# Kernel optimization log

Hardware: AMD Instinct MI355X
Metric: run time of the kernel (lower is better)

## Reference

```python
import jax, jax.numpy as jnp
import numpy as np

# Constants matching init_kwargs
PC_MIN_X, PC_MIN_Y = -70.4, -40.0
VX, VY = 0.1, 0.1
RADII = (0.4, 0.8)
NSAMPLE = 16
EPS = 1e-5

B, K, N = 2, 2048, 16384
C_BEV, H_BEV, W_BEV = 256, 100, 176


def setup_inputs() -> dict:
    key = jax.random.key(0)
    ks = jax.random.split(key, 16)
    u = lambda k, s: jax.random.uniform(k, s, jnp.float32)
    kp = jnp.stack([
        u(ks[0], (B, K)) * 136.0 - 68.0,
        u(ks[1], (B, K)) * 76.0 - 38.0,
        u(ks[2], (B, K)) * 2.5 - 2.0,   # z in (-2.0, 0.5) -> kpt_mask all True
    ], axis=-1)
    pts = jnp.stack([
        u(ks[3], (B, N)) * 140.0 - 70.0,
        u(ks[4], (B, N)) * 80.0 - 40.0,
        u(ks[5], (B, N)) * 4.0 - 3.0,
    ], axis=-1)
    r = lambda k, s: jax.random.normal(k, s, jnp.float32)
    s01 = lambda k, s: r(k, s) * 0.1
    return {
        "keypoints": kp,
        "points_xyz": pts,
        "points_feat": r(ks[6], (B, N, 1)),
        "spatial_features": r(ks[7], (B, C_BEV, H_BEV, W_BEV)),
        "bev_stride": 8,
        "W0_s0": s01(ks[8], (16, 4)), "g0_s0": jnp.ones(16), "b0_s0": jnp.zeros(16),
        "W1_s0": s01(ks[9], (16, 16)), "g1_s0": jnp.ones(16), "b1_s0": jnp.zeros(16),
        "W0_s1": s01(ks[10], (16, 4)), "g0_s1": jnp.ones(16), "b0_s1": jnp.zeros(16),
        "W1_s1": s01(ks[11], (32, 16)), "g1_s1": jnp.ones(32), "b1_s1": jnp.zeros(32),
        "Wf": s01(ks[12], (128, 304)), "gf": jnp.ones(128), "bf": jnp.zeros(128),
    }


def _batchnorm(x, g, b, axes):
    m = x.mean(axes, keepdims=True)
    v = x.var(axes, keepdims=True)
    return (x - m) * jax.lax.rsqrt(v + EPS) * g + b


def _ball_group(dist2, xyz_b, feat_b, kp_b, radius, ns):
    """pcdet ball_query: first ns in-radius neighbors (index order), pad by first idx."""
    Kq, Np = dist2.shape
    within = dist2 < radius * radius                      # (K, N)
    order = jnp.cumsum(within, axis=1) - 1                # slot for each point
    valid = within & (order < ns)
    pos = jnp.where(valid, order, ns)                     # invalid -> overflow slot
    idx = jnp.zeros((Kq, ns + 1), jnp.int32)
    idx = idx.at[jnp.arange(Kq)[:, None], pos].set(
        jnp.broadcast_to(jnp.arange(Np, dtype=jnp.int32)[None, :], (Kq, Np)))
    idx = idx[:, :ns]
    cnt = within.sum(axis=1)
    slot_ok = jnp.arange(ns)[None, :] < cnt[:, None]
    idx = jnp.where(slot_ok, idx, idx[:, :1])             # replicate first found idx
    empty = cnt == 0
    grouped_xyz = xyz_b[idx] - kp_b[:, None, :]           # (K, ns, 3)
    grouped = jnp.concatenate([grouped_xyz, feat_b[idx]], axis=-1)  # (K, ns, 3+C)
    grouped = jnp.where(empty[:, None, None], 0.0, grouped)
    return grouped, empty


def _group_both_scales(xyz_b, feat_b, kp_b):
    # pairwise dist computed ONCE, shared across both radii
    dist2 = jnp.sum((kp_b[:, None, :] - xyz_b[None, :, :]) ** 2, axis=-1)  # (K, N)
    g0, e0 = _ball_group(dist2, xyz_b, feat_b, kp_b, RADII[0], NSAMPLE)
    g1, e1 = _ball_group(dist2, xyz_b, feat_b, kp_b, RADII[1], NSAMPLE)
    return g0, e0, g1, e1


def _shared_mlp_pool(grouped, empty, layers):
    x = grouped                                            # (B, K, ns, Cin)
    for (W, g, b) in layers:
        x = jnp.einsum('bknc,oc->bkno', x, W)
        x = _batchnorm(x, g, b, axes=(0, 1, 2))            # BN2d over stacked M*ns
        x = jax.nn.relu(x)
    pooled = x.max(axis=2)                                 # max over ns -> (B, K, Cout)
    return jnp.where(empty[:, :, None], 0.0, pooled)


def _bev_interp(bev, kp, stride):
    # bev: (B, C, H, W); kp: (B, K, 3)
    im = jnp.transpose(bev, (0, 2, 3, 1))                  # (B, H, W, C)
    x = (kp[..., 0] - PC_MIN_X) / VX / stride
    y = (kp[..., 1] - PC_MIN_Y) / VY / stride
    Hh, Ww = im.shape[1], im.shape[2]
    x0 = jnp.clip(jnp.floor(x).astype(jnp.int32), 0, Ww - 1)
    x1 = jnp.clip(jnp.floor(x).astype(jnp.int32) + 1, 0, Ww - 1)
    y0 = jnp.clip(jnp.floor(y).astype(jnp.int32), 0, Hh - 1)
    y1 = jnp.clip(jnp.floor(y).astype(jnp.int32) + 1, 0, Hh - 1)
    bidx = jnp.arange(im.shape[0])[:, None]
    Ia, Ib = im[bidx, y0, x0], im[bidx, y1, x0]
    Ic, Id = im[bidx, y0, x1], im[bidx, y1, x1]
    x0f, x1f = x0.astype(x.dtype), x1.astype(x.dtype)
    y0f, y1f = y0.astype(y.dtype), y1.astype(y.dtype)
    wa = ((x1f - x) * (y1f - y))[..., None]
    wb = ((x1f - x) * (y - y0f))[..., None]
    wc = ((x - x0f) * (y1f - y))[..., None]
    wd = ((x - x0f) * (y - y0f))[..., None]
    return Ia * wa + Ib * wb + Ic * wc + Id * wd           # (B, K, C)


def reference(keypoints, points_xyz, points_feat, spatial_features, bev_stride,
              W0_s0, g0_s0, b0_s0, W1_s0, g1_s0, b1_s0,
              W0_s1, g0_s1, b0_s1, W1_s1, g1_s1, b1_s1,
              Wf, gf, bf):
    Bb, Kk, _ = keypoints.shape
    # BEV bilinear interpolation
    bev_feat = _bev_interp(spatial_features, keypoints, bev_stride)  # (B, K, C_bev)
    # per-batch ball-query grouping (vmapped over batch)
    g0, e0, g1, e1 = jax.vmap(_group_both_scales)(points_xyz, points_feat, keypoints)
    p0 = _shared_mlp_pool(g0, e0, [(W0_s0, g0_s0, b0_s0), (W1_s0, g1_s0, b1_s0)])
    p1 = _shared_mlp_pool(g1, e1, [(W0_s1, g0_s1, b0_s1), (W1_s1, g1_s1, b1_s1)])
    pooled = jnp.concatenate([p0, p1], axis=-1)            # (B, K, 48)
    feats = jnp.concatenate([bev_feat, pooled], axis=-1).reshape(Bb * Kk, -1)  # (M, 304)
    # vsa_point_feature_fusion: Linear(no bias) + BN1d(train) + ReLU
    fused = feats @ Wf.T
    fused = jax.nn.relu(_batchnorm(fused, gf, bf, axes=(0,)))
    return fused                                           # (B*K, 128)
```

## Files before the change

kernel.cpp:

```cpp
#include <hip/hip_runtime.h>
#include <hip/hip_bf16.h>

#define NB    2
#define NK    2048
#define NPTS  16384
#define NBK   4096
#define MSAMP 65536.0f
#define MROW  4096.0f

#define NCELLX 176
#define NCELLY 101
#define NCELLS 17776
#define CAP    24
#define CANDMAX 64

#define NREP   32
#define NCTR   64

#define AL(p) __hip_atomic_load((p), __ATOMIC_RELAXED, __HIP_MEMORY_SCOPE_AGENT)

#define ATOMIC_ADD_ACK(p, v) do { \
  float _r = atomicAdd((p), (v)); \
  asm volatile("" :: "v"(_r)); } while (0)

#define ACC14(M, w, X, Y, Z, F) do { \
  M[0] += (w)*(X); M[1] += (w)*(Y); M[2] += (w)*(Z); M[3] += (w)*(F); \
  M[4] += (w)*(X)*(X); M[5] += (w)*(X)*(Y); M[6] += (w)*(X)*(Z); M[7] += (w)*(X)*(F); \
  M[8] += (w)*(Y)*(Y); M[9] += (w)*(Y)*(Z); M[10] += (w)*(Y)*(F); \
  M[11] += (w)*(Z)*(Z); M[12] += (w)*(Z)*(F); M[13] += (w)*(F)*(F); } while (0)

__device__ __forceinline__ int cell_of(float x, float y) {
  int cx = (int)floorf((x + 70.4f) * 1.25f);
  int cy = (int)floorf((y + 40.0f) * 1.25f);
  cx = min(max(cx, 0), NCELLX - 1);
  cy = min(max(cy, 0), NCELLY - 1);
  return cy * NCELLX + cx;
}

__device__ __forceinline__ void grid_barrier(int* base, int per, int myc) {
  asm volatile("s_waitcnt vmcnt(0)" ::: "memory");
  __syncthreads();
  const int t = threadIdx.x;
  int* ctr = base;
  int* rel = base + NCTR;
  if (t == 0) {
    int old = __hip_atomic_fetch_add(&ctr[myc], 1, __ATOMIC_RELAXED,
                                     __HIP_MEMORY_SCOPE_AGENT);
    asm volatile("" :: "v"(old));
  }
  if (blockIdx.x == 0) {
    if (t < NCTR) {
      while (AL(&ctr[t]) < per) __builtin_amdgcn_s_sleep(8);
    }
    __syncthreads();
    if (t < NCTR)
      __hip_atomic_store(&rel[t], 1, __ATOMIC_RELAXED,
                         __HIP_MEMORY_SCOPE_AGENT);
  } else {
    if (t == 0) {
      while (AL(&rel[myc]) == 0) __builtin_amdgcn_s_sleep(8);
    }
  }
  __syncthreads();
}

__global__ __launch_bounds__(256) void bintrans_kernel(
    const float* __restrict__ pts, const float* __restrict__ pfeat,
    const float* __restrict__ bev,
    int* __restrict__ cellcnt, float4* __restrict__ bucketP,
    int* __restrict__ bucketI, float* __restrict__ bevT)
{
  __shared__ __align__(16) float ttile[64][65];
  const int t = threadIdx.x;
  const int wave = t >> 6;
  const int lane = t & 63;

  if (blockIdx.x < 128) {
    const int i  = blockIdx.x * 256 + t;
    const int b  = i >> 14;
    const int il = i & (NPTS - 1);
    const float* px = pts + (size_t)b * NPTS * 3;
    const float x = px[il*3+0], y = px[il*3+1], z = px[il*3+2];
    const float f = pfeat[(size_t)b * NPTS + il];
    const int c = b * NCELLS + cell_of(x, y);
    const int pos = atomicAdd(&cellcnt[c], 1);
    if (pos < CAP) {
      bucketP[(size_t)c * CAP + pos] = make_float4(x, y, z, f);
      bucketI[(size_t)c * CAP + pos] = il;
    }
    return;
  }

  const int tb  = blockIdx.x - 128;
  const int b   = tb / 1100;
  const int rem = tb % 1100;
  const int cg  = (rem / 275) * 64;
  const int sp0 = (rem % 275) * 64;
  #pragma unroll 4
  for (int i = 0; i < 16; i++) {
    const int c = cg + wave * 16 + i;
    ttile[wave * 16 + i][lane] = bev[((size_t)(b * 256 + c)) * 17600 + sp0 + lane];
  }
  __syncthreads();
  #pragma unroll 4
  for (int i = 0; i < 16; i++) {
    const int s = wave * 16 + i;
    bevT[((size_t)b * 17600 + sp0 + s) * 256 + cg + lane] = ttile[lane][s];
  }
}

__global__ __launch_bounds__(256, 2) void fused_kernel(
    const float* __restrict__ kp, const int* __restrict__ stridep,
    const float* __restrict__ bevT,
    const int* __restrict__ cellcnt, const float4* __restrict__ bucketP,
    const int* __restrict__ bucketI,
    const float* __restrict__ W0s0, const float* __restrict__ gm0s0, const float* __restrict__ bt0s0,
    const float* __restrict__ W0s1, const float* __restrict__ gm0s1, const float* __restrict__ bt0s1,
    const float* __restrict__ W1s0, const float* __restrict__ gm1s0, const float* __restrict__ bt1s0,
    const float* __restrict__ W1s1, const float* __restrict__ gm1s1, const float* __restrict__ bt1s1,
    const float* __restrict__ Wf, const float* __restrict__ gf, const float* __restrict__ bfp,
    float* __restrict__ S0r, float* __restrict__ S1r,
    float* __restrict__ S2sr, float* __restrict__ S2qr,
    int* __restrict__ ctrs, float* __restrict__ out)
{
  __shared__ float sW0a[64], sW0b[64], sW1a[256], sW1b[512], sP[160];
  __shared__ float skp[24];
  __shared__ float red[8][96];
  __shared__ float t2s[2][128], t2q[2][128];
  __shared__ float sA[128], sB[128];
  __shared__ float s0p[8][28], sS0[28];
  __shared__ __align__(16) float sF[8 * 304];
  __shared__ float4 sG0[8][16], sG1[8][16];
  __shared__ __align__(16) float4 sCand[8][CANDMAX];
  __shared__ int sCandI[8][CANDMAX];
  __shared__ int sTot[8];
  __shared__ int scnt[2][8];
  const int t = threadIdx.x;
  const int bk0 = blockIdx.x * 8;
  const int rep = blockIdx.x & (NREP - 1);
  const int myc = blockIdx.x & (NCTR - 1);

  if (t < 24) skp[t] = kp[(size_t)bk0 * 3 + t];
  if (t < 64) { sW0a[t] = W0s0[t]; sW0b[t] = W0s1[t]; }
  sW1a[t]       = W1s0[t];
  sW1b[t]       = W1s1[t];
  sW1b[t + 256] = W1s1[t + 256];
  for (int i = t; i < 8 * 96; i += 256) ((float*)red)[i] = 0.f;
  __syncthreads();

  {
    const float st = (float)(*stridep);
    const int b = bk0 >> 11;
    const size_t pb = (size_t)b * 17600 * 256;
    #pragma unroll
    for (int r = 0; r < 8; r++) {
      const float x = (skp[r*3+0] - (-70.4f)) / 0.1f / st;
      const float y = (skp[r*3+1] - (-40.0f)) / 0.1f / st;
      const int xf = (int)floorf(x), yf = (int)floorf(y);
      const int x0 = min(max(xf, 0), 175), x1 = min(max(xf + 1, 0), 175);
      const int y0 = min(max(yf, 0), 99),  y1 = min(max(yf + 1, 0), 99);
      const float x0f = (float)x0, x1f = (float)x1, y0f = (float)y0, y1f = (float)y1;
      const float wa = (x1f - x) * (y1f - y);
      const float wb = (x1f - x) * (y - y0f);
      const float wc = (x - x0f) * (y1f - y);
      const float wd = (x - x0f) * (y - y0f);
      const float Ia = bevT[pb + (size_t)(y0 * 176 + x0) * 256 + t];
      const float Ib = bevT[pb + (size_t)(y1 * 176 + x0) * 256 + t];
      const float Ic = bevT[pb + (size_t)(y0 * 176 + x1) * 256 + t];
      const float Id = bevT[pb + (size_t)(y1 * 176 + x1) * 256 + t];
      sF[r * 304 + t] = Ia * wa + Ib * wb + Ic * wc + Id * wd;
    }
  }

  if (t < 64) {
    const int kpi = t >> 3, sub = t & 7;
    const int b   = (bk0 + kpi) >> 11;
    const float kx = skp[kpi*3+0], ky = skp[kpi*3+1];
    int cx = (int)floorf((kx + 70.4f) * 1.25f);
    int cy = (int)floorf((ky + 40.0f) * 1.25f);
    cx = min(max(cx, 1), NCELLX - 2);
    cy = min(max(cy, 1), NCELLY - 2);
    const int cb0 = b * NCELLS + (cy - 1) * NCELLX + cx - 1;
    const int cellS = cb0 + (sub / 3) * NCELLX + (sub % 3);
    const int cell8 = cb0 + 2 * NCELLX + 2;
    const int nS = min(cellcnt[cellS], CAP);
    const int n8 = (sub == 0) ? min(cellcnt[cell8], CAP) : 0;
    int pre = nS;
    #pragma unroll
    for (int d = 1; d < 8; d <<= 1) {
      const int v = __shfl_up(pre, d, 8);
      if (sub >= d) pre += v;
    }
    const int offS  = pre - nS;
    const int tot07 = __shfl(pre, 7, 8);
    const float4* bp = bucketP + (size_t)cellS * CAP;
    const int*    bi = bucketI + (size_t)cellS * CAP;
    for (int j = 0; j < nS; ++j) {
      const int o = offS + j;
      if (o < CANDMAX) { sCand[kpi][o] = bp[j]; sCandI[kpi][o] = bi[j]; }
    }
    if (sub == 0) {
      const float4* bp8 = bucketP + (size_t)cell8 * CAP;
      const int*    bi8 = bucketI + (size_t)cell8 * CAP;
      for (int j = 0; j < n8; ++j) {
        const int o = tot07 + j;
        if (o < CANDMAX) { sCand[kpi][o] = bp8[j]; sCandI[kpi][o] = bi8[j]; }
      }
      sTot[kpi] = min(tot07 + n8, CANDMAX);
    }
  }
  __syncthreads();

  if (t < 64 && (t & 7) == 0) {
    const int kpi = t >> 3;
    const float kx = skp[kpi*3+0], ky = skp[kpi*3+1], kz = skp[kpi*3+2];
    const int T = sTot[kpi];

    int c0 = 0, c1 = 0;
    int mi0 = 0x7fffffff, mi1 = 0x7fffffff;
    float p0x = 0.f, p0y = 0.f, p0z = 0.f, p0f = 0.f;
    float p1x = 0.f, p1y = 0.f, p1z = 0.f, p1f = 0.f;
    float M0[14], M1[14];
    #pragma unroll
    for (int i = 0; i < 14; i++) { M0[i] = 0.f; M1[i] = 0.f; }

    for (int j = 0; j < T; ++j) {
      const float4 p = sCand[kpi][j];
      const float dx = p.x - kx, dy = p.y - ky, dz = p.z - kz;
      const float d2 = dx*dx + dy*dy + dz*dz;
      if (d2 < 0.64f) {
        const int pi = sCandI[kpi][j];
        if (c1 < 16) {
          sG1[kpi][c1] = make_float4(dx, dy, dz, p.w);
          ACC14(M1, 1.0f, dx, dy, dz, p.w);
        }
        if (pi < mi1) { mi1 = pi; p1x = dx; p1y = dy; p1z = dz; p1f = p.w; }
        c1++;
        if (d2 < 0.16f) {
          if (c0 < 16) {
            sG0[kpi][c0] = make_float4(dx, dy, dz, p.w);
            ACC14(M0, 1.0f, dx, dy, dz, p.w);
          }
          if (pi < mi0) { mi0 = pi; p0x = dx; p0y = dy; p0z = dz; p0f = p.w; }
          c0++;
        }
      }
    }

    {
      const float4 v0 = make_float4(p0x, p0y, p0z, p0f);
      for (int s2 = c0; s2 < 16; ++s2) sG0[kpi][s2] = v0;
      const float w0 = (float)(16 - min(c0, 16));
      ACC14(M0, w0, p0x, p0y, p0z, p0f);
    }
    {
      const float4 v1 = make_float4(p1x, p1y, p1z, p1f);
      for (int s2 = c1; s2 < 16; ++s2) sG1[kpi][s2] = v1;
      const float w1 = (float)(16 - min(c1, 16));
      ACC14(M1, w1, p1x, p1y, p1z, p1f);
    }
    scnt[0][kpi] = c0;
    scnt[1][kpi] = c1;

    #pragma unroll
    for (int d = 8; d < 64; d <<= 1) {
      #pragma unroll
      for (int i = 0; i < 14; i++) {
        M0[i] += __shfl_xor(M0[i], d);
        M1[i] += __shfl_xor(M1[i], d);
      }
    }
    if (t == 0) {
      float* S0my = S0r + rep * 32;
      #pragma unroll
      for (int i = 0; i < 14; i++) {
        ATOMIC_ADD_ACK(&S0my[i],      M0[i]);
        ATOMIC_ADD_ACK(&S0my[14 + i], M1[i]);
      }
    }
  }

  grid_barrier(ctrs, 512 / NCTR, myc);

  if (t < 224) {
    const int m = t % 28, g = t / 28;
    float a = 0.f;
    #pragma unroll
    for (int r2 = 0; r2 < 4; r2++) a += AL(S0r + (g * 4 + r2) * 32 + m);
    s0p[g][m] = a;
  }
  __syncthreads();
  if (t < 28) {
    float a = 0.f;
    #pragma unroll
    for (int g = 0; g < 8; g++) a += s0p[g][t];
    sS0[t] = a;
  }
  __syncthreads();
  if (t < 32) {
    const int s = t >> 4, c = t & 15;
    const float* W  = s ? sW0b : sW0a;
    const float* G  = s ? gm0s1 : gm0s0;
    const float* Bt = s ? bt0s1 : bt0s0;
    const float* Sx = sS0 + s * 14;
    const float w0 = W[c*4+0], w1 = W[c*4+1];
    const float w2 = W[c*4+2], w3 = W[c*4+3];
    const float inv = 1.0f / MSAMP;
    const float mean = (w0*Sx[0] + w1*Sx[1] + w2*Sx[2] + w3*Sx[3]) * inv;
    float e2 = w0*w0*Sx[4] + 2.f*w0*w1*Sx[5] + 2.f*w0*w2*Sx[6] + 2.f*w0*w3*Sx[7]
             + w1*w1*Sx[8] + 2.f*w1*w2*Sx[9] + 2.f*w1*w3*Sx[10]
             + w2*w2*Sx[11] + 2.f*w2*w3*Sx[12] + w3*w3*Sx[13];
    e2 *= inv;
    const float var = e2 - mean * mean;
    const float A = G[c] / sqrtf(var + 1e-5f);
    sP[s*32 + c]      = A;
    sP[s*32 + 16 + c] = Bt[c] - mean * A;
  }
  __syncthreads();

  float h2a[16], h2b[32];
  if (t < 128) {
    const int lkp = t >> 4, sl = t & 15;
    const int grp = t >> 4;
    const bool leader = (t & 15) == 0;
    float a1[16];
    {
      const float4 x = sG0[lkp][sl];
      #pragma unroll
      for (int c = 0; c < 16; c++) {
        const float h = sW0a[c*4+0]*x.x + sW0a[c*4+1]*x.y + sW0a[c*4+2]*x.z + sW0a[c*4+3]*x.w;
        a1[c] = fmaxf(fmaf(sP[c], h, sP[16+c]), 0.f);
      }
      #pragma unroll
      for (int o = 0; o < 16; o++) {
        float h2 = 0.f;
        #pragma unroll
        for (int c = 0; c < 16; c++) h2 = fmaf(sW1a[o*16+c], a1[c], h2);
        h2a[o] = h2;
        float s = h2, q = h2 * h2;
        #pragma unroll
        for (int d = 1; d < 16; d <<= 1) { s += __shfl_xor(s, d); q += __shfl_xor(q, d); }
        if (leader) { red[grp][o] += s; red[grp][16+o] += q; }
      }
    }
    {
      const float4 x = sG1[lkp][sl];
      #pragma unroll
      for (int c = 0; c < 16; c++) {
        const float h = sW0b[c*4+0]*x.x + sW0b[c*4+1]*x.y + sW0b[c*4+2]*x.z + sW0b[c*4+3]*x.w;
        a1[c] = fmaxf(fmaf(sP[32+c], h, sP[48+c]), 0.f);
      }
      #pragma unroll
      for (int o = 0; o < 32; o++) {
        float h2 = 0.f;
        #pragma unroll
        for (int c = 0; c < 16; c++) h2 = fmaf(sW1b[o*16+c], a1[c], h2);
        h2b[o] = h2;
        float s = h2, q = h2 * h2;
        #pragma unroll
        for (int d = 1; d < 16; d <<= 1) { s += __shfl_xor(s, d); q += __shfl_xor(q, d); }
        if (leader) { red[grp][32+o] += s; red[grp][64+o] += q; }
      }
    }
  }
  __syncthreads();
  if (t < 96) {
    float s = 0.f;
    #pragma unroll
    for (int g = 0; g < 8; g++) s += red[g][t];
    ATOMIC_ADD_ACK(&S1r[rep * 96 + t], s);
  }

  grid_barrier(ctrs + 2 * NCTR, 512 / NCTR, myc);

  if (t < 192) {
    const int v = t % 96, h = t / 96;
    float a = 0.f;
    #pragma unroll
    for (int r2 = 0; r2 < 16; r2++) a += AL(S1r + (h * 16 + r2) * 96 + v);
    red[h][v] = a;
  }
  __syncthreads();
  if (t < 48) {
    float sum, sq, G, Bv; int oA, oB, os, oq;
    if (t < 16) { os = t; oq = 16 + t; G = gm1s0[t]; Bv = bt1s0[t]; oA = 64+t;  oB = 80+t; }
    else { const int c = t - 16; os = 32 + c; oq = 64 + c; G = gm1s1[c]; Bv = bt1s1[c]; oA = 96+c; oB = 128+c; }
    sum = red[0][os] + red[1][os];
    sq  = red[0][oq] + red[1][oq];
    const float mean = sum / MSAMP;
    const float var  = sq / MSAMP - mean * mean;
    const float A = G / sqrtf(var + 1e-5f);
    sP[oA] = A;
    sP[oB] = Bv - mean * A;
  }
  __syncthreads();

  if (t < 128) {
    const int lkp = t >> 4, slot = t & 15;
    float a2s0[16], a2s1[32];
    #pragma unroll
    for (int o = 0; o < 16; o++) a2s0[o] = fmaxf(fmaf(sP[64+o], h2a[o], sP[80+o]), 0.f);
    #pragma unroll
    for (int o = 0; o < 32; o++) a2s1[o] = fmaxf(fmaf(sP[96+o], h2b[o], sP[128+o]), 0.f);
    #pragma unroll
    for (int d = 1; d < 16; d <<= 1) {
      #pragma unroll
      for (int o = 0; o < 16; o++) a2s0[o] = fmaxf(a2s0[o], __shfl_xor(a2s0[o], d));
      #pragma unroll
      for (int o = 0; o < 32; o++) a2s1[o] = fmaxf(a2s1[o], __shfl_xor(a2s1[o], d));
    }
    if (slot == 0) {
      const int c0 = scnt[0][lkp], c1 = scnt[1][lkp];
      float* outp = sF + lkp * 304 + 256;
      #pragma unroll
      for (int o = 0; o < 16; o++) outp[o] = c0 ? a2s0[o] : 0.f;
      #pragma unroll
      for (int o = 0; o < 32; o++) outp[16 + o] = c1 ? a2s1[o] : 0.f;
    }
  }
  __syncthreads();

  const int c = t & 127;
  const int half = t >> 7;
  const int rbase = half * 4;
  float acc[4];
  {
    #pragma unroll
    for (int r = 0; r < 4; r++) acc[r] = 0.f;
    const float* wrow = Wf + (size_t)c * 304;
    for (int j4 = 0; j4 < 76; j4++) {
      const float4 w = *(const float4*)(wrow + j4 * 4);
      #pragma unroll
      for (int r = 0; r < 4; r++) {
        const float4 f = *(const float4*)(sF + (rbase + r) * 304 + j4 * 4);
        acc[r] = fmaf(w.x, f.x, acc[r]);
        acc[r] = fmaf(w.y, f.y, acc[r]);
        acc[r] = fmaf(w.z, f.z, acc[r]);
        acc[r] = fmaf(w.w, f.w, acc[r]);
      }
    }
    float s = 0.f, q = 0.f;
    #pragma unroll
    for (int r = 0; r < 4; r++) {
      s += acc[r];
      q = fmaf(acc[r], acc[r], q);
    }
    t2s[half][c] = s;
    t2q[half][c] = q;
  }
  __syncthreads();
  if (t < 128) {
    ATOMIC_ADD_ACK(&S2sr[rep * 128 + t], t2s[0][t] + t2s[1][t]);
    ATOMIC_ADD_ACK(&S2qr[rep * 128 + t], t2q[0][t] + t2q[1][t]);
  }

  grid_barrier(ctrs + 4 * NCTR, 512 / NCTR, myc);

  {
    const int v = t & 127;
    const float* Sx = (t < 128) ? S2sr : S2qr;
    float a = 0.f;
    #pragma unroll
    for (int r = 0; r < NREP; r++) a += AL(Sx + r * 128 + v);
    if (t < 128) t2s[0][v] = a; else t2q[0][v] = a;
  }
  __syncthreads();
  if (t < 128) {
    const float mean = t2s[0][t] / MROW;
    const float var  = t2q[0][t] / MROW - mean * mean;
    const float A = gf[t] / sqrtf(var + 1e-5f);
    sA[t] = A;
    sB[t] = bfp[t] - mean * A;
  }
  __syncthreads();
  {
    const float A = sA[c], B = sB[c];
    #pragma unroll
    for (int r = 0; r < 4; r++) {
      out[(size_t)(bk0 + rbase + r) * 128 + c] = fmaxf(fmaf(acc[r], A, B), 0.f);
    }
  }
}

extern "C" void kernel_launch(void* const* d_in, const int* in_sizes, int n_in,
                              void* d_out, int out_size, void* d_ws, size_t ws_size,
                              hipStream_t stream)
{
  const float* kp    = (const float*)d_in[0];
  const float* pts   = (const float*)d_in[1];
  const float* pfeat = (const float*)d_in[2];
  const float* bev   = (const float*)d_in[3];
  const int*   strd  = (const int*)d_in[4];
  const float* W0s0  = (const float*)d_in[5];
  const float* g0s0  = (const float*)d_in[6];
  const float* b0s0  = (const float*)d_in[7];
  const float* W1s0  = (const float*)d_in[8];
  const float* g1s0  = (const float*)d_in[9];
  const float* b1s0  = (const float*)d_in[10];
  const float* W0s1  = (const float*)d_in[11];
  const float* g0s1  = (const float*)d_in[12];
  const float* b0s1  = (const float*)d_in[13];
  const float* W1s1  = (const float*)d_in[14];
  const float* g1s1  = (const float*)d_in[15];
  const float* b1s1  = (const float*)d_in[16];
  const float* Wf    = (const float*)d_in[17];
  const float* gf    = (const float*)d_in[18];
  const float* bfv   = (const float*)d_in[19];

  float* w = (float*)d_ws;
  int*   cellcnt = (int*)(w + 1048576);
  int*   ctrs    = cellcnt + 2 * NCELLS;
  float* S0r     = (float*)(ctrs + 6 * NCTR);
  float* S1r     = S0r + NREP * 32;
  float* S2sr    = S1r + NREP * 96;
  float* S2qr    = S2sr + NREP * 128;
  const size_t zero_elems = 2 * NCELLS + 6 * NCTR
                          + NREP * (32 + 96 + 128 + 128);

  float*  bevT    = w + 1245184;
  float4* bucketP = (float4*)(w + 10256384);
  int*    bucketI = (int*)(w + 10256384 + (size_t)2 * NCELLS * CAP * 4);

  hipMemsetAsync(cellcnt, 0, zero_elems * sizeof(int), stream);
  hipLaunchKernelGGL(bintrans_kernel, dim3(2328), dim3(256), 0, stream,
                     pts, pfeat, bev, cellcnt, bucketP, bucketI, bevT);
  hipLaunchKernelGGL(fused_kernel, dim3(512), dim3(256), 0, stream,
                     kp, strd, bevT, cellcnt, bucketP, bucketI,
                     W0s0, g0s0, b0s0, W0s1, g0s1, b0s1,
                     W1s0, g1s0, b1s0, W1s1, g1s1, b1s1,
                     Wf, gf, bfv, S0r, S1r, S2sr, S2qr, ctrs, (float*)d_out);
}
```

Baseline: 183.8 us.

## Fold point binning and BEV gather into fused kernel, drop BEV transpose

Removes the separate bintrans kernel. The full BEV tensor transpose (about 36 MB read and written) is replaced by direct strided gathers from the original channel-major layout. Point binning now happens inside the fused kernel: 64 threads per block each bin one point, using atomic exchanges so the writes are visible across the GPU, and an extra grid barrier follows before ball-query use. This saves a launch and heavy memory traffic, at the cost of uncoalesced bilinear gathers (each thread reads a different channel plane) and one more grid-wide sync.

After: 205.6 us. 11.8% more time.

```diff
diff --git a/kernel.cpp b/kernel.cpp
--- a/kernel.cpp
+++ b/kernel.cpp
@@ -64,56 +64,12 @@
   __syncthreads();
 }
 
-__global__ __launch_bounds__(256) void bintrans_kernel(
-    const float* __restrict__ pts, const float* __restrict__ pfeat,
-    const float* __restrict__ bev,
+__global__ __launch_bounds__(256, 2) void fused_kernel(
+    const float* __restrict__ kp, const float* __restrict__ pts,
+    const float* __restrict__ pfeat, const float* __restrict__ bev,
+    const int* __restrict__ stridep,
     int* __restrict__ cellcnt, float4* __restrict__ bucketP,
-    int* __restrict__ bucketI, float* __restrict__ bevT)
-{
-  __shared__ __align__(16) float ttile[64][65];
-  const int t = threadIdx.x;
-  const int wave = t >> 6;
-  const int lane = t & 63;
-
-  if (blockIdx.x < 128) {
-    const int i  = blockIdx.x * 256 + t;
-    const int b  = i >> 14;
-    const int il = i & (NPTS - 1);
-    const float* px = pts + (size_t)b * NPTS * 3;
-    const float x = px[il*3+0], y = px[il*3+1], z = px[il*3+2];
-    const float f = pfeat[(size_t)b * NPTS + il];
-    const int c = b * NCELLS + cell_of(x, y);
-    const int pos = atomicAdd(&cellcnt[c], 1);
-    if (pos < CAP) {
-      bucketP[(size_t)c * CAP + pos] = make_float4(x, y, z, f);
-      bucketI[(size_t)c * CAP + pos] = il;
-    }
-    return;
-  }
-
-  const int tb  = blockIdx.x - 128;
-  const int b   = tb / 1100;
-  const int rem = tb % 1100;
-  const int cg  = (rem / 275) * 64;
-  const int sp0 = (rem % 275) * 64;
-  #pragma unroll 4
-  for (int i = 0; i < 16; i++) {
-    const int c = cg + wave * 16 + i;
-    ttile[wave * 16 + i][lane] = bev[((size_t)(b * 256 + c)) * 17600 + sp0 + lane];
-  }
-  __syncthreads();
-  #pragma unroll 4
-  for (int i = 0; i < 16; i++) {
-    const int s = wave * 16 + i;
-    bevT[((size_t)b * 17600 + sp0 + s) * 256 + cg + lane] = ttile[lane][s];
-  }
-}
-
-__global__ __launch_bounds__(256, 2) void fused_kernel(
-    const float* __restrict__ kp, const int* __restrict__ stridep,
-    const float* __restrict__ bevT,
-    const int* __restrict__ cellcnt, const float4* __restrict__ bucketP,
-    const int* __restrict__ bucketI,
+    int* __restrict__ bucketI,
     const float* __restrict__ W0s0, const float* __restrict__ gm0s0, const float* __restrict__ bt0s0,
     const float* __restrict__ W0s1, const float* __restrict__ gm0s1, const float* __restrict__ bt0s1,
     const float* __restrict__ W1s0, const float* __restrict__ gm1s0, const float* __restrict__ bt1s0,
@@ -151,7 +107,7 @@
   {
     const float st = (float)(*stridep);
     const int b = bk0 >> 11;
-    const size_t pb = (size_t)b * 17600 * 256;
+    const size_t cb = ((size_t)(b * 256 + t)) * 17600;
     #pragma unroll
     for (int r = 0; r < 8; r++) {
       const float x = (skp[r*3+0] - (-70.4f)) / 0.1f / st;
@@ -164,13 +120,39 @@
       const float wb = (x1f - x) * (y - y0f);
       const float wc = (x - x0f) * (y1f - y);
       const float wd = (x - x0f) * (y - y0f);
-      const float Ia = bevT[pb + (size_t)(y0 * 176 + x0) * 256 + t];
-      const float Ib = bevT[pb + (size_t)(y1 * 176 + x0) * 256 + t];
-      const float Ic = bevT[pb + (size_t)(y0 * 176 + x1) * 256 + t];
-      const float Id = bevT[pb + (size_t)(y1 * 176 + x1) * 256 + t];
+      const float Ia = bev[cb + y0 * 176 + x0];
+      const float Ib = bev[cb + y1 * 176 + x0];
+      const float Ic = bev[cb + y0 * 176 + x1];
+      const float Id = bev[cb + y1 * 176 + x1];
       sF[r * 304 + t] = Ia * wa + Ib * wb + Ic * wc + Id * wd;
     }
   }
+
+  if (t < 64) {
+    const int i  = blockIdx.x * 64 + t;
+    const int b  = i >> 14;
+    const int il = i & (NPTS - 1);
+    const float* px = pts + (size_t)b * NPTS * 3;
+    const float x = px[il*3+0], y = px[il*3+1], z = px[il*3+2];
+    const float f = pfeat[(size_t)b * NPTS + il];
+    const int c = b * NCELLS + cell_of(x, y);
+    const int pos = atomicAdd(&cellcnt[c], 1);
+    if (pos < CAP) {
+      union { float4 v; unsigned long long u[2]; } pk;
+      pk.v = make_float4(x, y, z, f);
+      unsigned long long* dst =
+          (unsigned long long*)&bucketP[(size_t)c * CAP + pos];
+      unsigned long long r0 = __hip_atomic_exchange(dst,     pk.u[0],
+          __ATOMIC_RELAXED, __HIP_MEMORY_SCOPE_AGENT);
+      unsigned long long r1 = __hip_atomic_exchange(dst + 1, pk.u[1],
+          __ATOMIC_RELAXED, __HIP_MEMORY_SCOPE_AGENT);
+      int r2 = __hip_atomic_exchange(&bucketI[(size_t)c * CAP + pos], il,
+          __ATOMIC_RELAXED, __HIP_MEMORY_SCOPE_AGENT);
+      asm volatile("" :: "v"(r0), "v"(r1), "v"(r2));
+    }
+  }
+
+  grid_barrier(ctrs, 512 / NCTR, myc);
 
   if (t < 64) {
     const int kpi = t >> 3, sub = t & 7;
@@ -280,7 +262,7 @@
     }
   }
 
-  grid_barrier(ctrs, 512 / NCTR, myc);
+  grid_barrier(ctrs + 2 * NCTR, 512 / NCTR, myc);
 
   if (t < 224) {
     const int m = t % 28, g = t / 28;
@@ -371,7 +353,7 @@
     ATOMIC_ADD_ACK(&S1r[rep * 96 + t], s);
   }
 
-  grid_barrier(ctrs + 2 * NCTR, 512 / NCTR, myc);
+  grid_barrier(ctrs + 4 * NCTR, 512 / NCTR, myc);
 
   if (t < 192) {
     const int v = t % 96, h = t / 96;
@@ -454,7 +436,7 @@
     ATOMIC_ADD_ACK(&S2qr[rep * 128 + t], t2q[0][t] + t2q[1][t]);
   }
 
-  grid_barrier(ctrs + 4 * NCTR, 512 / NCTR, myc);
+  grid_barrier(ctrs + 6 * NCTR, 512 / NCTR, myc);
 
   {
     const int v = t & 127;
@@ -510,22 +492,20 @@
   float* w = (float*)d_ws;
   int*   cellcnt = (int*)(w + 1048576);
   int*   ctrs    = cellcnt + 2 * NCELLS;
-  float* S0r     = (float*)(ctrs + 6 * NCTR);
+  float* S0r     = (float*)(ctrs + 8 * NCTR);
   float* S1r     = S0r + NREP * 32;
   float* S2sr    = S1r + NREP * 96;
   float* S2qr    = S2sr + NREP * 128;
-  const size_t zero_elems = 2 * NCELLS + 6 * NCTR
+  const size_t zero_elems = 2 * NCELLS + 8 * NCTR
                           + NREP * (32 + 96 + 128 + 128);
 
-  float*  bevT    = w + 1245184;
-  float4* bucketP = (float4*)(w + 10256384);
-  int*    bucketI = (int*)(w + 10256384 + (size_t)2 * NCELLS * CAP * 4);
+  float4* bucketP = (float4*)(w + 1245184);
+  int*    bucketI = (int*)(w + 1245184 + (size_t)2 * NCELLS * CAP * 4);
 
   hipMemsetAsync(cellcnt, 0, zero_elems * sizeof(int), stream);
-  hipLaunchKernelGGL(bintrans_kernel, dim3(2328), dim3(256), 0, stream,
-                     pts, pfeat, bev, cellcnt, bucketP, bucketI, bevT);
   hipLaunchKernelGGL(fused_kernel, dim3(512), dim3(256), 0, stream,
-                     kp, strd, bevT, cellcnt, bucketP, bucketI,
+                     kp, pts, pfeat, bev, strd,
+                     cellcnt, bucketP, bucketI,
                      W0s0, g0s0, b0s0, W0s1, g0s1, b0s1,
                      W1s0, g1s0, b1s0, W1s1, g1s1, b1s1,
                      Wf, gf, bfv, S0r, S1r, S2sr, S2qr, ctrs, (float*)d_out);
```

## Replace memset with in-kernel zeroing and move point binning into fused kernel

Applied to the files above, without the earlier changes.

The hipMemsetAsync is replaced by zeroing blocks inside the transpose kernel, which removes one launch. Point binning moves from the first kernel into the fused kernel, where 64 threads per block bin points using atomic exchanges so the writes are visible device-wide. An extra grid barrier is added before the ball query can read the buckets. This trades one launch and memset for an additional grid-wide synchronization and shifts the binning work onto the critical path of the fused kernel.

New measurement: 189.9 us. +3.3%, slower.

```diff
diff --git a/kernel.cpp b/kernel.cpp
--- a/kernel.cpp
+++ b/kernel.cpp
@@ -16,6 +16,8 @@
 
 #define NREP   32
 #define NCTR   64
+#define ZELEMS (2 * NCELLS + 8 * NCTR + NREP * (32 + 96 + 128 + 128))
+#define ZBLOCKS 189
 
 #define AL(p) __hip_atomic_load((p), __ATOMIC_RELAXED, __HIP_MEMORY_SCOPE_AGENT)
 
@@ -64,34 +66,22 @@
   __syncthreads();
 }
 
-__global__ __launch_bounds__(256) void bintrans_kernel(
-    const float* __restrict__ pts, const float* __restrict__ pfeat,
-    const float* __restrict__ bev,
-    int* __restrict__ cellcnt, float4* __restrict__ bucketP,
-    int* __restrict__ bucketI, float* __restrict__ bevT)
+__global__ __launch_bounds__(256) void transzero_kernel(
+    const float* __restrict__ bev, float* __restrict__ bevT,
+    int* __restrict__ zbase)
 {
   __shared__ __align__(16) float ttile[64][65];
   const int t = threadIdx.x;
   const int wave = t >> 6;
   const int lane = t & 63;
 
-  if (blockIdx.x < 128) {
-    const int i  = blockIdx.x * 256 + t;
-    const int b  = i >> 14;
-    const int il = i & (NPTS - 1);
-    const float* px = pts + (size_t)b * NPTS * 3;
-    const float x = px[il*3+0], y = px[il*3+1], z = px[il*3+2];
-    const float f = pfeat[(size_t)b * NPTS + il];
-    const int c = b * NCELLS + cell_of(x, y);
-    const int pos = atomicAdd(&cellcnt[c], 1);
-    if (pos < CAP) {
-      bucketP[(size_t)c * CAP + pos] = make_float4(x, y, z, f);
-      bucketI[(size_t)c * CAP + pos] = il;
-    }
+  if (blockIdx.x < ZBLOCKS) {
+    const int i = blockIdx.x * 256 + t;
+    if (i < ZELEMS) zbase[i] = 0;
     return;
   }
 
-  const int tb  = blockIdx.x - 128;
+  const int tb  = blockIdx.x - ZBLOCKS;
   const int b   = tb / 1100;
   const int rem = tb % 1100;
   const int cg  = (rem / 275) * 64;
@@ -110,10 +100,11 @@
 }
 
 __global__ __launch_bounds__(256, 2) void fused_kernel(
-    const float* __restrict__ kp, const int* __restrict__ stridep,
-    const float* __restrict__ bevT,
-    const int* __restrict__ cellcnt, const float4* __restrict__ bucketP,
-    const int* __restrict__ bucketI,
+    const float* __restrict__ kp, const float* __restrict__ pts,
+    const float* __restrict__ pfeat, const float* __restrict__ bevT,
+    const int* __restrict__ stridep,
+    int* __restrict__ cellcnt, float4* __restrict__ bucketP,
+    int* __restrict__ bucketI,
     const float* __restrict__ W0s0, const float* __restrict__ gm0s0, const float* __restrict__ bt0s0,
     const float* __restrict__ W0s1, const float* __restrict__ gm0s1, const float* __restrict__ bt0s1,
     const float* __restrict__ W1s0, const float* __restrict__ gm1s0, const float* __restrict__ bt1s0,
@@ -173,6 +164,32 @@
   }
 
   if (t < 64) {
+    const int i  = blockIdx.x * 64 + t;
+    const int b  = i >> 14;
+    const int il = i & (NPTS - 1);
+    const float* px = pts + (size_t)b * NPTS * 3;
+    const float x = px[il*3+0], y = px[il*3+1], z = px[il*3+2];
+    const float f = pfeat[(size_t)b * NPTS + il];
+    const int c = b * NCELLS + cell_of(x, y);
+    const int pos = atomicAdd(&cellcnt[c], 1);
+    if (pos < CAP) {
+      union { float4 v; unsigned long long u[2]; } pk;
+      pk.v = make_float4(x, y, z, f);
+      unsigned long long* dst =
+          (unsigned long long*)&bucketP[(size_t)c * CAP + pos];
+      unsigned long long r0 = __hip_atomic_exchange(dst,     pk.u[0],
+          __ATOMIC_RELAXED, __HIP_MEMORY_SCOPE_AGENT);
+      unsigned long long r1 = __hip_atomic_exchange(dst + 1, pk.u[1],
+          __ATOMIC_RELAXED, __HIP_MEMORY_SCOPE_AGENT);
+      int r2 = __hip_atomic_exchange(&bucketI[(size_t)c * CAP + pos], il,
+          __ATOMIC_RELAXED, __HIP_MEMORY_SCOPE_AGENT);
+      asm volatile("" :: "v"(r0), "v"(r1), "v"(r2));
+    }
+  }
+
+  grid_barrier(ctrs, 512 / NCTR, myc);
+
+  if (t < 64) {
     const int kpi = t >> 3, sub = t & 7;
     const int b   = (bk0 + kpi) >> 11;
     const float kx = skp[kpi*3+0], ky = skp[kpi*3+1];
@@ -280,7 +297,7 @@
     }
   }
 
-  grid_barrier(ctrs, 512 / NCTR, myc);
+  grid_barrier(ctrs + 2 * NCTR, 512 / NCTR, myc);
 
   if (t < 224) {
     const int m = t % 28, g = t / 28;
@@ -371,7 +388,7 @@
     ATOMIC_ADD_ACK(&S1r[rep * 96 + t], s);
   }
 
-  grid_barrier(ctrs + 2 * NCTR, 512 / NCTR, myc);
+  grid_barrier(ctrs + 4 * NCTR, 512 / NCTR, myc);
 
   if (t < 192) {
     const int v = t % 96, h = t / 96;
@@ -454,7 +471,7 @@
     ATOMIC_ADD_ACK(&S2qr[rep * 128 + t], t2q[0][t] + t2q[1][t]);
   }
 
-  grid_barrier(ctrs + 4 * NCTR, 512 / NCTR, myc);
+  grid_barrier(ctrs + 6 * NCTR, 512 / NCTR, myc);
 
   {
     const int v = t & 127;
@@ -510,22 +527,20 @@
   float* w = (float*)d_ws;
   int*   cellcnt = (int*)(w + 1048576);
   int*   ctrs    = cellcnt + 2 * NCELLS;
-  float* S0r     = (float*)(ctrs + 6 * NCTR);
+  float* S0r     = (float*)(ctrs + 8 * NCTR);
   float* S1r     = S0r + NREP * 32;
   float* S2sr    = S1r + NREP * 96;
   float* S2qr    = S2sr + NREP * 128;
-  const size_t zero_elems = 2 * NCELLS + 6 * NCTR
-                          + NREP * (32 + 96 + 128 + 128);
 
   float*  bevT    = w + 1245184;
   float4* bucketP = (float4*)(w + 10256384);
   int*    bucketI = (int*)(w + 10256384 + (size_t)2 * NCELLS * CAP * 4);
 
-  hipMemsetAsync(cellcnt, 0, zero_elems * sizeof(int), stream);
-  hipLaunchKernelGGL(bintrans_kernel, dim3(2328), dim3(256), 0, stream,
-                     pts, pfeat, bev, cellcnt, bucketP, bucketI, bevT);
+  hipLaunchKernelGGL(transzero_kernel, dim3(ZBLOCKS + 2200), dim3(256), 0,
+                     stream, bev, bevT, cellcnt);
   hipLaunchKernelGGL(fused_kernel, dim3(512), dim3(256), 0, stream,
-                     kp, strd, bevT, cellcnt, bucketP, bucketI,
+                     kp, pts, pfeat, bevT, strd,
+                     cellcnt, bucketP, bucketI,
                      W0s0, g0s0, b0s0, W0s1, g0s1, b0s1,
                      W1s0, g1s0, b1s0, W1s1, g1s1, b1s1,
                      Wf, gf, bfv, S0r, S1r, S2sr, S2qr, ctrs, (float*)d_out);
```
